# Performance work log

Measured on AMD Instinct MI355X. Metric: run time of the kernel, lower is better.

Reference implementation:

```python
import jax, jax.numpy as jnp
import numpy as np

N, E = 100000, 1600000
IN, HID, EMB = 128, 256, 64


def setup_inputs() -> dict:
    key = jax.random.key(0)
    ks = jax.random.split(key, 8)
    x = jax.random.normal(ks[0], (N, IN), dtype=jnp.float32)
    edge_index = jax.random.randint(ks[1], (2, E), 0, N, dtype=jnp.int64)
    def glorot(k, fan_in, fan_out):
        lim = np.sqrt(6.0 / (fan_in + fan_out)).astype(np.float32)
        return jax.random.uniform(k, (fan_in, fan_out), jnp.float32, -lim, lim)
    return {
        "x": x,
        "edge_index": edge_index,
        "W1": glorot(ks[2], IN, HID), "b1": jnp.zeros((HID,), jnp.float32),
        "W2": glorot(ks[3], HID, HID), "b2": jnp.zeros((HID,), jnp.float32),
        "W3": glorot(ks[4], HID, EMB), "b3": jnp.zeros((EMB,), jnp.float32),
    }


def reference(x, edge_index, W1, b1, W2, b2, W3, b3):
    n = x.shape[0]
    # add self loops (PyG GCNConv default, fill_value=1)
    loops = jnp.arange(n, dtype=edge_index.dtype)
    src = jnp.concatenate([edge_index[0], loops])
    dst = jnp.concatenate([edge_index[1], loops])
    # symmetric normalization D^-1/2 A_hat D^-1/2 (degree at target)
    deg = jax.ops.segment_sum(jnp.ones_like(src, dtype=x.dtype), dst, num_segments=n)
    dinv = jnp.where(deg > 0, deg ** -0.5, 0.0)
    norm = (dinv[src] * dinv[dst])[:, None]  # [E+N, 1]

    def conv(h, W, b):
        h = h @ W                               # [N, out]
        agg = jax.ops.segment_sum(h[src] * norm, dst, num_segments=n)
        return agg + b

    h = jax.nn.relu(conv(x, W1, b1))   # dropout: identity in eval mode
    h = jax.nn.relu(conv(h, W2, b2))
    h = conv(h, W3, b3)
    # L2-normalize rows (F.normalize, eps=1e-12)
    nrm = jnp.linalg.norm(h, axis=1, keepdims=True)
    return h / jnp.maximum(nrm, 1e-12)
```

## Files before the change

### kernel.cpp

```cpp
#include <hip/hip_runtime.h>
#include <cstddef>
#include <cstdint>

constexpr int IN_F  = 128;
constexpr int HID_F = 256;
constexpr int EMB_F = 64;

typedef float  f32x4  __attribute__((ext_vector_type(4)));
typedef short  bf16x8 __attribute__((ext_vector_type(8)));
typedef unsigned short ushort_t;
typedef ushort_t u16x8 __attribute__((ext_vector_type(8)));
typedef ushort_t u16x4 __attribute__((ext_vector_type(4)));

__device__ inline float bf2f(ushort_t u) {
  union { unsigned i; float f; } c; c.i = ((unsigned)u) << 16; return c.f;
}
__device__ inline ushort_t f2bf(float f) {
  union { float f; unsigned i; } c; c.f = f;
  unsigned r = c.i + 0x7FFFu + ((c.i >> 16) & 1u);
  return (ushort_t)(r >> 16);
}

constexpr int NBKT = 512;
constexpr int CHUNK = 16384;


__global__ void k_setup(const float* __restrict__ W1, const float* __restrict__ W2,
                        const float* __restrict__ W3,
                        ushort_t* __restrict__ W1t, ushort_t* __restrict__ W2t,
                        ushort_t* __restrict__ W3t, int* __restrict__ ghist) {
  constexpr int c1 = IN_F * HID_F;
  constexpr int c2 = c1 + HID_F * HID_F;
  constexpr int c3 = c2 + HID_F * EMB_F;
  int i = blockIdx.x * blockDim.x + threadIdx.x;
  if (i < c1) {
    int k = i / HID_F, nn = i - k * HID_F;
    W1t[(size_t)nn * IN_F + k] = f2bf(W1[i]);
  } else if (i < c2) {
    int j = i - c1;
    int k = j / HID_F, nn = j - k * HID_F;
    W2t[(size_t)nn * HID_F + k] = f2bf(W2[j]);
  } else if (i < c3) {
    int j = i - c2;
    int k = j / EMB_F, nn = j - k * EMB_F;
    W3t[(size_t)nn * HID_F + k] = f2bf(W3[j]);
  } else if (i - c3 < NBKT) {
    ghist[i - c3] = 0;
  }
}


__global__ __launch_bounds__(512) void k_hist(const int* __restrict__ dst,
                                              int* __restrict__ ghist, int e) {
  __shared__ int cnt[NBKT];
  cnt[threadIdx.x] = 0;
  __syncthreads();
  int i0 = blockIdx.x * CHUNK;
  int i1 = min(e, i0 + CHUNK);
  for (int i = i0 + threadIdx.x; i < i1; i += 512)
    atomicAdd(&cnt[dst[i] >> 8], 1);
  __syncthreads();
  int c = cnt[threadIdx.x];
  if (c > 0) atomicAdd(&ghist[threadIdx.x], c);
}

__global__ __launch_bounds__(512) void k_bscan(const int* __restrict__ ghist,
                                               int* __restrict__ bstart,
                                               int* __restrict__ gcursor) {
  __shared__ int s[NBKT];
  int v = ghist[threadIdx.x];
  s[threadIdx.x] = v;
  __syncthreads();
#pragma unroll
  for (int off = 1; off < NBKT; off <<= 1) {
    int t = (threadIdx.x >= off) ? s[threadIdx.x - off] : 0;
    __syncthreads();
    s[threadIdx.x] += t;
    __syncthreads();
  }
  int ex = s[threadIdx.x] - v;
  bstart[threadIdx.x] = ex;
  gcursor[threadIdx.x] = ex;
}

__global__ __launch_bounds__(512) void k_passA(const int* __restrict__ src,
                                               const int* __restrict__ dst,
                                               int* __restrict__ gcursor,
                                               unsigned* __restrict__ staged, int e) {
  __shared__ int cnt[NBKT];
  __shared__ int base[NBKT];
  cnt[threadIdx.x] = 0;
  __syncthreads();
  int i0 = blockIdx.x * CHUNK;
  int i1 = min(e, i0 + CHUNK);
  for (int i = i0 + threadIdx.x; i < i1; i += 512)
    atomicAdd(&cnt[dst[i] >> 8], 1);
  __syncthreads();
  int c = cnt[threadIdx.x];
  base[threadIdx.x] = (c > 0) ? atomicAdd(&gcursor[threadIdx.x], c) : 0;
  cnt[threadIdx.x] = 0;
  __syncthreads();
  for (int i = i0 + threadIdx.x; i < i1; i += 512) {
    int d = dst[i];
    int b = d >> 8;
    int lp = atomicAdd(&cnt[b], 1);
    staged[base[b] + lp] = ((unsigned)(d & 255) << 17) | (unsigned)src[i];
  }
}

__global__ __launch_bounds__(256) void k_Bfused(
    const unsigned* __restrict__ staged, const int* __restrict__ bstart,
    const int* __restrict__ ghist, const float* __restrict__ x,
    float* __restrict__ dinv, int* __restrict__ rowptr, int* __restrict__ csr,
    ushort_t* __restrict__ xb, int n, int e) {
  __shared__ int cnt[256];
  __shared__ int s[256];
  __shared__ int cur[256];
  __shared__ float dinvL[256];
  const int tid = threadIdx.x;
  const int b = blockIdx.x;
  cnt[tid] = 0;
  __syncthreads();
  const int beg = bstart[b], end = beg + ghist[b];
  for (int i = beg + tid; i < end; i += 256)
    atomicAdd(&cnt[staged[i] >> 17], 1);
  __syncthreads();
  const int node = (b << 8) + tid;
  int v = (node < n) ? cnt[tid] : 0;
  float dv = rsqrtf((float)(v + 1));
  if (node < n) { dinv[node] = dv; }
  dinvL[tid] = dv;
  s[tid] = v;
  __syncthreads();
#pragma unroll
  for (int off = 1; off < 256; off <<= 1) {
    int t = (tid >= off) ? s[tid - off] : 0;
    __syncthreads();
    s[tid] += t;
    __syncthreads();
  }
  int rp = beg + s[tid] - v;
  if (node < n) rowptr[node] = rp;
  if (b == 0 && tid == 0) rowptr[n] = e;
  cur[tid] = rp;
  __syncthreads();
  for (int i = beg + tid; i < end; i += 256) {
    unsigned p = staged[i];
    int l = (int)(p >> 17);
    int sv = (int)(p & 0x1FFFFu);
    int pos = atomicAdd(&cur[l], 1);
    csr[pos] = sv;
  }
  const int nb0 = b << 8;
  const int rows = min(256, n - nb0);
  const float4* xv = reinterpret_cast<const float4*>(x) + (size_t)nb0 * 32;
  u16x4* xo = reinterpret_cast<u16x4*>(xb) + (size_t)nb0 * 32;
  for (int j = tid; j < rows * 32; j += 256) {
    float sc = dinvL[j >> 5];
    float4 vv = xv[j];
    u16x4 o;
    o[0] = f2bf(vv.x * sc); o[1] = f2bf(vv.y * sc);
    o[2] = f2bf(vv.z * sc); o[3] = f2bf(vv.w * sc);
    xo[j] = o;
  }
}


__global__ __launch_bounds__(256) void k_gather1(
    const ushort_t* __restrict__ t, ushort_t* __restrict__ outp,
    const int* __restrict__ rowptr, const int* __restrict__ csr, int n) {
  int wid = (blockIdx.x * blockDim.x + threadIdx.x) >> 6;
  int lane = threadIdx.x & 63;
  if (wid >= n) return;
  const int half = lane >> 5, sub = lane & 31;
  const int coff = sub * 4;
  int beg = rowptr[wid], end = rowptr[wid + 1];
  int nitems = end - beg + 1;
  float acc[4] = {};
  int i = 0;
  for (; i + 3 < nitems; i += 4) {
    int i0 = i + half, i1 = i + 2 + half;
    int r0 = (i0 == 0) ? wid : csr[beg + i0 - 1];
    int r1 = csr[beg + i1 - 1];
    u16x4 v0 = *reinterpret_cast<const u16x4*>(t + (size_t)r0 * IN_F + coff);
    u16x4 v1 = *reinterpret_cast<const u16x4*>(t + (size_t)r1 * IN_F + coff);
#pragma unroll
    for (int k = 0; k < 4; ++k) acc[k] += bf2f(v0[k]);
#pragma unroll
    for (int k = 0; k < 4; ++k) acc[k] += bf2f(v1[k]);
  }
  for (; i < nitems; i += 2) {
    int i0 = i + half;
    if (i0 < nitems) {
      int r0 = (i0 == 0) ? wid : csr[beg + i0 - 1];
      u16x4 v0 = *reinterpret_cast<const u16x4*>(t + (size_t)r0 * IN_F + coff);
#pragma unroll
      for (int k = 0; k < 4; ++k) acc[k] += bf2f(v0[k]);
    }
  }
#pragma unroll
  for (int k = 0; k < 4; ++k) acc[k] += __shfl_xor(acc[k], 32);
  if (half == 0) {
    u16x4 o;
#pragma unroll
    for (int k = 0; k < 4; ++k) o[k] = f2bf(acc[k]);
    *reinterpret_cast<u16x4*>(outp + (size_t)wid * IN_F + coff) = o;
  }
}

__global__ __launch_bounds__(256) void k_gather2(
    const ushort_t* __restrict__ t, ushort_t* __restrict__ outp,
    const int* __restrict__ rowptr, const int* __restrict__ csr,
    const float* __restrict__ dinv, const float* __restrict__ bias, int n) {
  int wid = (blockIdx.x * blockDim.x + threadIdx.x) >> 6;
  int lane = threadIdx.x & 63;
  if (wid >= n) return;
  const int half = lane >> 5, sub = lane & 31;
  const int coff = sub * 8;
  int beg = rowptr[wid], end = rowptr[wid + 1];
  int nitems = end - beg + 1;
  float acc[8] = {};
  int i = 0;
  for (; i + 3 < nitems; i += 4) {
    int i0 = i + half, i1 = i + 2 + half;
    int r0 = (i0 == 0) ? wid : csr[beg + i0 - 1];
    int r1 = csr[beg + i1 - 1];
    u16x8 v0 = *reinterpret_cast<const u16x8*>(t + (size_t)r0 * HID_F + coff);
    u16x8 v1 = *reinterpret_cast<const u16x8*>(t + (size_t)r1 * HID_F + coff);
#pragma unroll
    for (int k = 0; k < 8; ++k) acc[k] += bf2f(v0[k]);
#pragma unroll
    for (int k = 0; k < 8; ++k) acc[k] += bf2f(v1[k]);
  }
  for (; i < nitems; i += 2) {
    int i0 = i + half;
    if (i0 < nitems) {
      int r0 = (i0 == 0) ? wid : csr[beg + i0 - 1];
      u16x8 v0 = *reinterpret_cast<const u16x8*>(t + (size_t)r0 * HID_F + coff);
#pragma unroll
      for (int k = 0; k < 8; ++k) acc[k] += bf2f(v0[k]);
    }
  }
#pragma unroll
  for (int k = 0; k < 8; ++k) acc[k] += __shfl_xor(acc[k], 32);
  if (half == 0) {
    float s = dinv[wid];
    u16x8 o;
#pragma unroll
    for (int k = 0; k < 8; ++k) o[k] = f2bf(fmaxf(fmaf(acc[k], s, bias[coff + k]), 0.f));
    *reinterpret_cast<u16x8*>(outp + (size_t)wid * HID_F + coff) = o;
  }
}

__global__ __launch_bounds__(256) void k_gather3(
    const ushort_t* __restrict__ t, float* __restrict__ outp,
    const int* __restrict__ rowptr, const int* __restrict__ csr,
    const float* __restrict__ dinv, const float* __restrict__ b3, int n) {
  int wid = (blockIdx.x * blockDim.x + threadIdx.x) >> 6;
  int lane = threadIdx.x & 63;
  if (wid >= n) return;
  const int q = lane >> 4, sub = lane & 15;
  const int coff = sub * 4;
  int beg = rowptr[wid], end = rowptr[wid + 1];
  int nitems = end - beg + 1;
  float acc[4] = {};
  for (int i = 0; i < nitems; i += 4) {
    int i0 = i + q;
    if (i0 < nitems) {
      int r0 = (i0 == 0) ? wid : csr[beg + i0 - 1];
      u16x4 v0 = *reinterpret_cast<const u16x4*>(t + (size_t)r0 * EMB_F + coff);
#pragma unroll
      for (int k = 0; k < 4; ++k) acc[k] += bf2f(v0[k]);
    }
  }
#pragma unroll
  for (int k = 0; k < 4; ++k) acc[k] += __shfl_xor(acc[k], 16);
#pragma unroll
  for (int k = 0; k < 4; ++k) acc[k] += __shfl_xor(acc[k], 32);
  float s = dinv[wid];
  float v[4], ss = 0.f;
#pragma unroll
  for (int k = 0; k < 4; ++k) {
    v[k] = fmaf(acc[k], s, b3[coff + k]);
    ss = fmaf(v[k], v[k], ss);
  }
#pragma unroll
  for (int off = 8; off > 0; off >>= 1) ss += __shfl_xor(ss, off);
  float inv = 1.0f / fmaxf(sqrtf(ss), 1e-12f);
  if (lane < 16) {
    float4 o = make_float4(v[0] * inv, v[1] * inv, v[2] * inv, v[3] * inv);
    *reinterpret_cast<float4*>(outp + (size_t)wid * EMB_F + coff) = o;
  }
}


template<int K, bool RELU>
__global__ __launch_bounds__(256) void k_gemm_big(
    const ushort_t* __restrict__ A, const ushort_t* __restrict__ Wt,
    ushort_t* __restrict__ C, const float* __restrict__ dinv,
    const float* __restrict__ bias, int M) {
  __shared__ ushort_t As[64 * K];
  const int tid = threadIdx.x;
  const int lane = tid & 63;
  const int w = tid >> 6;
  const int mbase = blockIdx.x * 64;

  constexpr int CH = K / 8;
  for (int i = tid; i < 64 * CH; i += 256) {
    int row = i / CH, c = i - row * CH;
    int g = mbase + row;
    if (g >= M) g = M - 1;
    u16x8 v = *reinterpret_cast<const u16x8*>(A + (size_t)g * K + c * 8);
    *reinterpret_cast<u16x8*>(&As[row * K + ((c ^ (row & 7)) << 3)]) = v;
  }
  __syncthreads();

  const int lrow = lane & 15;
  const int lk = (lane >> 4) * 8;
  const int nbase = w * 64;
  f32x4 acc[4][4] = {};

#pragma unroll
  for (int k0 = 0; k0 < K; k0 += 32) {
    bf16x8 a[4], b[4];
    const int cbase = (k0 >> 3) + (lane >> 4);
#pragma unroll
    for (int i = 0; i < 4; ++i) {
      int ri = i * 16 + lrow;
      a[i] = *reinterpret_cast<const bf16x8*>(&As[ri * K + ((cbase ^ (ri & 7)) << 3)]);
    }
#pragma unroll
    for (int n = 0; n < 4; ++n)
      b[n] = *reinterpret_cast<const bf16x8*>(Wt + (size_t)(nbase + n * 16 + lrow) * K + k0 + lk);
#pragma unroll
    for (int i = 0; i < 4; ++i)
#pragma unroll
      for (int n = 0; n < 4; ++n)
        acc[i][n] = __builtin_amdgcn_mfma_f32_16x16x32_bf16(a[i], b[n], acc[i][n], 0, 0, 0);
  }

#pragma unroll
  for (int i = 0; i < 4; ++i) {
    int growb = mbase + i * 16 + (lane >> 4) * 4;
#pragma unroll
    for (int r = 0; r < 4; ++r) {
      int grow = growb + r;
      if (grow >= M) continue;
      float s = dinv[grow];
#pragma unroll
      for (int n = 0; n < 4; ++n) {
        int gcol = nbase + n * 16 + (lane & 15);
        float v = acc[i][n][r] * s;
        if (RELU) v = fmaxf(v + bias[gcol], 0.f);
        C[(size_t)grow * HID_F + gcol] = f2bf(v);
      }
    }
  }
}


template<int K, bool RELU>
__global__ __launch_bounds__(256) void k_mfma_gemm(
    const ushort_t* __restrict__ A, const ushort_t* __restrict__ Wt,
    ushort_t* __restrict__ C,
    const float* __restrict__ dinv, const float* __restrict__ bias,
    int M, int NT ) {
  int w = blockIdx.x * 4 + (threadIdx.x >> 6);
  int lane = threadIdx.x & 63;
  int mt = w / NT, nt = w - mt * NT;
  int mbase = mt * 64, nbase = nt * 64;
  if (mbase >= M) return;
  const int lrow = lane & 15;
  const int lk = (lane >> 4) * 8;
  const int N = NT * 64;

  int rows[4];
#pragma unroll
  for (int i = 0; i < 4; ++i) {
    int r = mbase + i * 16 + lrow;
    rows[i] = (r < M) ? r : (M - 1);
  }

  f32x4 acc[4][4] = {};

#pragma unroll 2
  for (int k0 = 0; k0 < K; k0 += 32) {
    bf16x8 a[4], b[4];
#pragma unroll
    for (int i = 0; i < 4; ++i)
      a[i] = *reinterpret_cast<const bf16x8*>(A + (size_t)rows[i] * K + k0 + lk);
#pragma unroll
    for (int n = 0; n < 4; ++n)
      b[n] = *reinterpret_cast<const bf16x8*>(Wt + (size_t)(nbase + n * 16 + lrow) * K + k0 + lk);
#pragma unroll
    for (int i = 0; i < 4; ++i)
#pragma unroll
      for (int n = 0; n < 4; ++n)
        acc[i][n] = __builtin_amdgcn_mfma_f32_16x16x32_bf16(a[i], b[n], acc[i][n], 0, 0, 0);
  }

#pragma unroll
  for (int i = 0; i < 4; ++i) {
    int growb = mbase + i * 16 + (lane >> 4) * 4;
#pragma unroll
    for (int r = 0; r < 4; ++r) {
      int grow = growb + r;
      if (grow >= M) continue;
      float s = dinv[grow];
#pragma unroll
      for (int n = 0; n < 4; ++n) {
        int gcol = nbase + n * 16 + (lane & 15);
        float v = acc[i][n][r] * s;
        if (RELU) v = fmaxf(v + bias[gcol], 0.f);
        C[(size_t)grow * N + gcol] = f2bf(v);
      }
    }
  }
}


extern "C" void kernel_launch(void* const* d_in, const int* in_sizes, int n_in,
                              void* d_out, int out_size, void* d_ws, size_t ws_size,
                              hipStream_t stream) {
  const float* x  = (const float*)d_in[0];
  const int*   ei = (const int*)d_in[1];
  const float* W1 = (const float*)d_in[2];
  const float* b1 = (const float*)d_in[3];
  const float* W2 = (const float*)d_in[4];
  const float* b2 = (const float*)d_in[5];
  const float* W3 = (const float*)d_in[6];
  const float* b3 = (const float*)d_in[7];
  const int N = in_sizes[0] / IN_F;
  const int E = in_sizes[1] / 2;
  const int* src = ei;
  const int* dst = ei + E;

  char* m = (char*)d_ws;
  auto alloc = [&](size_t bytes) { char* p = m; m += (bytes + 255) & ~(size_t)255; return p; };
  ushort_t* U1  = (ushort_t*)alloc((size_t)N * HID_F * 2);
  ushort_t* U2  = (ushort_t*)alloc((size_t)N * HID_F * 2);
  ushort_t* W1t = (ushort_t*)alloc((size_t)IN_F * HID_F * 2);
  ushort_t* W2t = (ushort_t*)alloc((size_t)HID_F * HID_F * 2);
  ushort_t* W3t = (ushort_t*)alloc((size_t)HID_F * EMB_F * 2);
  float*    dinv    = (float*)alloc((size_t)N * 4);
  int*      rowptr  = (int*)alloc((size_t)(N + 1) * 4);
  int*      ghist   = (int*)alloc(NBKT * 4);
  int*      bstart  = (int*)alloc(NBKT * 4);
  int*      gcursor = (int*)alloc(NBKT * 4);
  unsigned* staged  = (unsigned*)alloc((size_t)E * 4);
  int*      csr     = (int*)alloc((size_t)E * 4);
  float*    out     = (float*)d_out;

  const int nb = (N + 255) / 256;
  const int echunks = (E + CHUNK - 1) / CHUNK;
  constexpr int SETUP_W = IN_F * HID_F + HID_F * HID_F + HID_F * EMB_F + NBKT;

  k_setup<<<(SETUP_W + 255) / 256, 256, 0, stream>>>(W1, W2, W3, W1t, W2t, W3t, ghist);

  k_hist  <<<echunks, 512, 0, stream>>>(dst, ghist, E);
  k_bscan <<<1, NBKT, 0, stream>>>(ghist, bstart, gcursor);
  k_passA <<<echunks, 512, 0, stream>>>(src, dst, gcursor, staged, E);

  ushort_t* xb = U2;
  k_Bfused<<<nb, 256, 0, stream>>>(staged, bstart, ghist, x, dinv, rowptr, csr, xb, N, E);

  const int gblocks = (N + 3) / 4;
  const int MT = (N + 63) / 64;

  ushort_t* aggX = U2 + (size_t)N * IN_F;
  k_gather1<<<gblocks, 256, 0, stream>>>(xb, aggX, rowptr, csr, N);
  ushort_t* h1 = U1;
  k_gemm_big<IN_F, true><<<MT, 256, 0, stream>>>(aggX, W1t, h1, dinv, b1, N);

  ushort_t* t2 = U2;
  k_gemm_big<HID_F, false><<<MT, 256, 0, stream>>>(h1, W2t, t2, dinv, nullptr, N);
  ushort_t* h2 = U1;
  k_gather2<<<gblocks, 256, 0, stream>>>(t2, h2, rowptr, csr, dinv, b2, N);

  ushort_t* t3 = U2;
  k_mfma_gemm<HID_F, false><<<(MT * (EMB_F / 64) + 3) / 4, 256, 0, stream>>>(
      h2, W3t, t3, dinv, nullptr, N, EMB_F / 64);
  k_gather3<<<gblocks, 256, 0, stream>>>(t3, out, rowptr, csr, dinv, b3, N);
}
```

Baseline: 435.8 us.

## Stage GEMM epilogues through LDS for coalesced stores and fuse setup into histogram

The GEMM epilogues now write bf16 results into a swizzled shared-memory tile and then store full 16-byte rows to global memory, replacing scattered 2-byte stores. The swizzle pattern changes to reduce bank conflicts, and the big GEMM always allocates a 64x256 tile so the output can reuse it. Weight transposition is merged into the histogram kernel as extra blocks, and ghist zeroing becomes a memset, which removes a launch. This costs extra shared-memory traffic and barriers, and the K=128 GEMM now uses more LDS, which may lower occupancy.

```diff
diff --git a/kernel.cpp b/kernel.cpp
--- a/kernel.cpp
+++ b/kernel.cpp
@@ -23,35 +23,35 @@
 
 constexpr int NBKT = 512;
 constexpr int CHUNK = 16384;
-
-
-__global__ void k_setup(const float* __restrict__ W1, const float* __restrict__ W2,
-                        const float* __restrict__ W3,
-                        ushort_t* __restrict__ W1t, ushort_t* __restrict__ W2t,
-                        ushort_t* __restrict__ W3t, int* __restrict__ ghist) {
-  constexpr int c1 = IN_F * HID_F;
-  constexpr int c2 = c1 + HID_F * HID_F;
-  constexpr int c3 = c2 + HID_F * EMB_F;
-  int i = blockIdx.x * blockDim.x + threadIdx.x;
-  if (i < c1) {
-    int k = i / HID_F, nn = i - k * HID_F;
-    W1t[(size_t)nn * IN_F + k] = f2bf(W1[i]);
-  } else if (i < c2) {
-    int j = i - c1;
-    int k = j / HID_F, nn = j - k * HID_F;
-    W2t[(size_t)nn * HID_F + k] = f2bf(W2[j]);
-  } else if (i < c3) {
-    int j = i - c2;
-    int k = j / EMB_F, nn = j - k * EMB_F;
-    W3t[(size_t)nn * HID_F + k] = f2bf(W3[j]);
-  } else if (i - c3 < NBKT) {
-    ghist[i - c3] = 0;
-  }
-}
-
-
-__global__ __launch_bounds__(512) void k_hist(const int* __restrict__ dst,
-                                              int* __restrict__ ghist, int e) {
+constexpr int SETUP_W = IN_F * HID_F + HID_F * HID_F + HID_F * EMB_F;
+constexpr int SETUP_BLOCKS = (SETUP_W + 511) / 512;
+
+
+__global__ __launch_bounds__(512) void k_histsetup(
+    const int* __restrict__ dst, int* __restrict__ ghist, int e, int echunks,
+    const float* __restrict__ W1, const float* __restrict__ W2,
+    const float* __restrict__ W3,
+    ushort_t* __restrict__ W1t, ushort_t* __restrict__ W2t,
+    ushort_t* __restrict__ W3t) {
+  if ((int)blockIdx.x >= echunks) {
+    constexpr int c1 = IN_F * HID_F;
+    constexpr int c2 = c1 + HID_F * HID_F;
+    constexpr int c3 = c2 + HID_F * EMB_F;
+    int i = ((int)blockIdx.x - echunks) * 512 + threadIdx.x;
+    if (i < c1) {
+      int k = i / HID_F, nn = i - k * HID_F;
+      W1t[(size_t)nn * IN_F + k] = f2bf(W1[i]);
+    } else if (i < c2) {
+      int j = i - c1;
+      int k = j / HID_F, nn = j - k * HID_F;
+      W2t[(size_t)nn * HID_F + k] = f2bf(W2[j]);
+    } else if (i < c3) {
+      int j = i - c2;
+      int k = j / EMB_F, nn = j - k * EMB_F;
+      W3t[(size_t)nn * HID_F + k] = f2bf(W3[j]);
+    }
+    return;
+  }
   __shared__ int cnt[NBKT];
   cnt[threadIdx.x] = 0;
   __syncthreads();
@@ -293,13 +293,15 @@
   }
 }
 
+__device__ inline int swz(int row) { return (row ^ (row >> 3)) & 7; }
+
 
 template<int K, bool RELU>
 __global__ __launch_bounds__(256) void k_gemm_big(
     const ushort_t* __restrict__ A, const ushort_t* __restrict__ Wt,
     ushort_t* __restrict__ C, const float* __restrict__ dinv,
     const float* __restrict__ bias, int M) {
-  __shared__ ushort_t As[64 * K];
+  __shared__ ushort_t As[64 * 256];
   const int tid = threadIdx.x;
   const int lane = tid & 63;
   const int w = tid >> 6;
@@ -311,7 +313,7 @@
     int g = mbase + row;
     if (g >= M) g = M - 1;
     u16x8 v = *reinterpret_cast<const u16x8*>(A + (size_t)g * K + c * 8);
-    *reinterpret_cast<u16x8*>(&As[row * K + ((c ^ (row & 7)) << 3)]) = v;
+    *reinterpret_cast<u16x8*>(&As[row * K + ((c ^ swz(row)) << 3)]) = v;
   }
   __syncthreads();
 
@@ -327,7 +329,7 @@
 #pragma unroll
     for (int i = 0; i < 4; ++i) {
       int ri = i * 16 + lrow;
-      a[i] = *reinterpret_cast<const bf16x8*>(&As[ri * K + ((cbase ^ (ri & 7)) << 3)]);
+      a[i] = *reinterpret_cast<const bf16x8*>(&As[ri * K + ((cbase ^ swz(ri)) << 3)]);
     }
 #pragma unroll
     for (int n = 0; n < 4; ++n)
@@ -339,40 +341,50 @@
         acc[i][n] = __builtin_amdgcn_mfma_f32_16x16x32_bf16(a[i], b[n], acc[i][n], 0, 0, 0);
   }
 
+  __syncthreads();
 #pragma unroll
   for (int i = 0; i < 4; ++i) {
-    int growb = mbase + i * 16 + (lane >> 4) * 4;
 #pragma unroll
     for (int r = 0; r < 4; ++r) {
-      int grow = growb + r;
-      if (grow >= M) continue;
-      float s = dinv[grow];
+      int row = i * 16 + (lane >> 4) * 4 + r;
+      int grow = mbase + row;
+      float s = (grow < M) ? dinv[grow] : 0.f;
+      int sw = swz(row);
 #pragma unroll
       for (int n = 0; n < 4; ++n) {
-        int gcol = nbase + n * 16 + (lane & 15);
+        int col = nbase + n * 16 + (lane & 15);
         float v = acc[i][n][r] * s;
-        if (RELU) v = fmaxf(v + bias[gcol], 0.f);
-        C[(size_t)grow * HID_F + gcol] = f2bf(v);
+        if (RELU) v = fmaxf(v + bias[col], 0.f);
+        As[row * 256 + (((col >> 3) ^ sw) << 3) + (col & 7)] = f2bf(v);
       }
     }
   }
-}
-
-
-template<int K, bool RELU>
-__global__ __launch_bounds__(256) void k_mfma_gemm(
+  __syncthreads();
+#pragma unroll
+  for (int p = 0; p < 8; ++p) {
+    int idx = p * 256 + tid;
+    int row = idx >> 5, c = idx & 31;
+    int grow = mbase + row;
+    if (grow < M) {
+      u16x8 v = *reinterpret_cast<const u16x8*>(&As[row * 256 + ((c ^ swz(row)) << 3)]);
+      *reinterpret_cast<u16x8*>(&C[(size_t)grow * 256 + c * 8]) = v;
+    }
+  }
+}
+
+
+__global__ __launch_bounds__(256) void k_gemm3(
     const ushort_t* __restrict__ A, const ushort_t* __restrict__ Wt,
-    ushort_t* __restrict__ C,
-    const float* __restrict__ dinv, const float* __restrict__ bias,
-    int M, int NT ) {
-  int w = blockIdx.x * 4 + (threadIdx.x >> 6);
-  int lane = threadIdx.x & 63;
-  int mt = w / NT, nt = w - mt * NT;
-  int mbase = mt * 64, nbase = nt * 64;
+    ushort_t* __restrict__ C, const float* __restrict__ dinv, int M) {
+  __shared__ ushort_t Cs[4 * 64 * 64];
+  constexpr int K = HID_F;
+  const int w = blockIdx.x * 4 + (threadIdx.x >> 6);
+  const int lane = threadIdx.x & 63;
+  const int mbase = w * 64;
   if (mbase >= M) return;
   const int lrow = lane & 15;
   const int lk = (lane >> 4) * 8;
-  const int N = NT * 64;
+  ushort_t* cs = &Cs[(threadIdx.x >> 6) * 4096];
 
   int rows[4];
 #pragma unroll
@@ -391,7 +403,7 @@
       a[i] = *reinterpret_cast<const bf16x8*>(A + (size_t)rows[i] * K + k0 + lk);
 #pragma unroll
     for (int n = 0; n < 4; ++n)
-      b[n] = *reinterpret_cast<const bf16x8*>(Wt + (size_t)(nbase + n * 16 + lrow) * K + k0 + lk);
+      b[n] = *reinterpret_cast<const bf16x8*>(Wt + (size_t)(n * 16 + lrow) * K + k0 + lk);
 #pragma unroll
     for (int i = 0; i < 4; ++i)
 #pragma unroll
@@ -401,19 +413,27 @@
 
 #pragma unroll
   for (int i = 0; i < 4; ++i) {
-    int growb = mbase + i * 16 + (lane >> 4) * 4;
 #pragma unroll
     for (int r = 0; r < 4; ++r) {
-      int grow = growb + r;
-      if (grow >= M) continue;
-      float s = dinv[grow];
+      int row = i * 16 + (lane >> 4) * 4 + r;
+      int grow = mbase + row;
+      float s = (grow < M) ? dinv[grow] : 0.f;
+      int sw = swz(row);
 #pragma unroll
       for (int n = 0; n < 4; ++n) {
-        int gcol = nbase + n * 16 + (lane & 15);
-        float v = acc[i][n][r] * s;
-        if (RELU) v = fmaxf(v + bias[gcol], 0.f);
-        C[(size_t)grow * N + gcol] = f2bf(v);
+        int col = n * 16 + (lane & 15);
+        cs[row * 64 + (((col >> 3) ^ sw) << 3) + (col & 7)] = f2bf(acc[i][n][r] * s);
       }
+    }
+  }
+#pragma unroll
+  for (int p = 0; p < 8; ++p) {
+    int idx = p * 64 + lane;
+    int row = idx >> 3, c = idx & 7;
+    int grow = mbase + row;
+    if (grow < M) {
+      u16x8 v = *reinterpret_cast<const u16x8*>(&cs[row * 64 + ((c ^ swz(row)) << 3)]);
+      *reinterpret_cast<u16x8*>(&C[(size_t)grow * 64 + c * 8]) = v;
     }
   }
 }
@@ -453,11 +473,11 @@
 
   const int nb = (N + 255) / 256;
   const int echunks = (E + CHUNK - 1) / CHUNK;
-  constexpr int SETUP_W = IN_F * HID_F + HID_F * HID_F + HID_F * EMB_F + NBKT;
-
-  k_setup<<<(SETUP_W + 255) / 256, 256, 0, stream>>>(W1, W2, W3, W1t, W2t, W3t, ghist);
-
-  k_hist  <<<echunks, 512, 0, stream>>>(dst, ghist, E);
+
+  hipMemsetAsync(ghist, 0, NBKT * 4, stream);
+
+  k_histsetup<<<echunks + SETUP_BLOCKS, 512, 0, stream>>>(
+      dst, ghist, E, echunks, W1, W2, W3, W1t, W2t, W3t);
   k_bscan <<<1, NBKT, 0, stream>>>(ghist, bstart, gcursor);
   k_passA <<<echunks, 512, 0, stream>>>(src, dst, gcursor, staged, E);
 
@@ -478,7 +498,6 @@
   k_gather2<<<gblocks, 256, 0, stream>>>(t2, h2, rowptr, csr, dinv, b2, N);
 
   ushort_t* t3 = U2;
-  k_mfma_gemm<HID_F, false><<<(MT * (EMB_F / 64) + 3) / 4, 256, 0, stream>>>(
-      h2, W3t, t3, dinv, nullptr, N, EMB_F / 64);
+  k_gemm3<<<(MT + 3) / 4, 256, 0, stream>>>(h2, W3t, t3, dinv, N);
   k_gather3<<<gblocks, 256, 0, stream>>>(t3, out, rowptr, csr, dinv, b3, N);
 }
```

Result: no change. 436.6 us (+0.2%).
